# Performance work log

Hardware: AMD Instinct MI355X
Metric: run time of the kernel (lower is better)

Reference implementation:

```python
import jax, jax.numpy as jnp
import numpy as np

L, B, T, C, H, V = 4, 4, 1024, 1024, 16, 32000
DH = C // H
FF = 4 * C
IGNORE = 5
EPS = 1e-5


def setup_inputs() -> dict:
    key = jax.random.key(0)
    ks = jax.random.split(key, 12)
    s = 0.02
    return {
        "idx": jax.random.randint(ks[0], (B, T), 0, V),
        "targets": jax.random.randint(ks[1], (B, T), 0, V),
        "tok_emb": jax.random.normal(ks[2], (V, C), jnp.float32) * s,
        "pos_emb": jax.random.normal(ks[3], (T, C), jnp.float32) * s,
        "Wq": jax.random.normal(ks[4], (L, C, C), jnp.float32) * s,
        "Wk": jax.random.normal(ks[5], (L, C, C), jnp.float32) * s,
        "Wv": jax.random.normal(ks[6], (L, C, C), jnp.float32) * s,
        "Wo": jax.random.normal(ks[7], (L, C, C), jnp.float32) * s,
        "bo": jnp.zeros((L, C), jnp.float32),
        "ln1_g": jnp.ones((L, C), jnp.float32),
        "ln1_b": jnp.zeros((L, C), jnp.float32),
        "ln2_g": jnp.ones((L, C), jnp.float32),
        "ln2_b": jnp.zeros((L, C), jnp.float32),
        "W1": jax.random.normal(ks[8], (L, C, FF), jnp.float32) * s,
        "b1": jnp.zeros((L, FF), jnp.float32),
        "W2": jax.random.normal(ks[9], (L, FF, C), jnp.float32) * s,
        "b2": jnp.zeros((L, C), jnp.float32),
        "lnf_g": jnp.ones((C,), jnp.float32),
        "lnf_b": jnp.zeros((C,), jnp.float32),
        "Whead": jax.random.normal(ks[10], (C, V), jnp.float32) * s,
        "bhead": jnp.zeros((V,), jnp.float32),
    }


def _layernorm(x, g, b):
    mu = jnp.mean(x, axis=-1, keepdims=True)
    var = jnp.var(x, axis=-1, keepdims=True)
    return (x - mu) * jax.lax.rsqrt(var + EPS) * g + b


def _gpt_forward(idx, targets, tok_emb, pos_emb, Wq, Wk, Wv, Wo, bo,
                 ln1_g, ln1_b, ln2_g, ln2_b, W1, b1, W2, b2,
                 lnf_g, lnf_b, Whead, bhead):
    x = tok_emb[idx] + pos_emb[None, :, :]  # [B,T,C]
    causal = jnp.tril(jnp.ones((T, T), bool))
    for i in range(L):
        h = _layernorm(x, ln1_g[i], ln1_b[i])
        q = (h @ Wq[i]).reshape(B, T, H, DH)
        k = (h @ Wk[i]).reshape(B, T, H, DH)
        v = (h @ Wv[i]).reshape(B, T, H, DH)
        wei = jnp.einsum("bqhd,bkhd->bhqk", q, k) * (DH ** -0.5)
        wei = jnp.where(causal[None, None], wei, -jnp.inf)
        wei = jax.nn.softmax(wei, axis=-1)
        att = jnp.einsum("bhqk,bkhd->bqhd", wei, v).reshape(B, T, C)
        x = x + att @ Wo[i] + bo[i]
        h = _layernorm(x, ln2_g[i], ln2_b[i])
        x = x + jax.nn.gelu(h @ W1[i] + b1[i], approximate=False) @ W2[i] + b2[i]
    x = _layernorm(x, lnf_g, lnf_b)
    logits = x @ Whead + bhead  # [B,T,V]
    # cross-entropy with ignore_index=5
    lg = logits.reshape(B * T, V)
    tg = targets.reshape(B * T)
    logp = jax.nn.log_softmax(lg, axis=-1)
    nll = -jnp.take_along_axis(logp, tg[:, None], axis=-1)[:, 0]
    valid = (tg != IGNORE).astype(lg.dtype)
    loss = jnp.sum(nll * valid) / jnp.maximum(jnp.sum(valid), 1.0)
    return logits, loss


def reference(idx, targets, tok_emb, pos_emb, Wq, Wk, Wv, Wo, bo,
              ln1_g, ln1_b, ln2_g, ln2_b, W1, b1, W2, b2,
              lnf_g, lnf_b, Whead, bhead):
    return _gpt_forward(idx, targets, tok_emb, pos_emb, Wq, Wk, Wv, Wo, bo,
                        ln1_g, ln1_b, ln2_g, ln2_b, W1, b1, W2, b2,
                        lnf_g, lnf_b, Whead, bhead)
```

## Files before the change

### kernel.cpp

```cpp
#include <hip/hip_runtime.h>
#include <cstdint>
#include <cstddef>

#define Lx 4
#define Bx 4
#define Tx 1024
#define Cx 1024
#define Hx 16
#define DHx 64
#define FFx 4096
#define Vx 32000
#define BTx 4096

typedef __attribute__((ext_vector_type(8))) __bf16 bf16x8;
typedef __attribute__((ext_vector_type(4))) float f32x4;
typedef __attribute__((ext_vector_type(8))) short short8;

__device__ __forceinline__ float bflo(unsigned u){ return __builtin_bit_cast(float, u << 16); }
__device__ __forceinline__ float bfhi(unsigned u){ return __builtin_bit_cast(float, u & 0xffff0000u); }
__device__ __forceinline__ float bf2f(short s){ return bflo((unsigned)(unsigned short)s); }
__device__ __forceinline__ short f2bf(float f){
  unsigned u = __builtin_bit_cast(unsigned, f);
  u += 0x7fffu + ((u >> 16) & 1u);
  return (short)(u >> 16);
}

__device__ __forceinline__ void gload_lds16(const short* g, short* l){
  __builtin_amdgcn_global_load_lds(
      (const __attribute__((address_space(1))) unsigned int*)g,
      (__attribute__((address_space(3))) unsigned int*)l, 16, 0, 0);
}

__device__ __forceinline__ int xcd_swizzle(int orig, int nwg){
  const int q = nwg >> 3, r = nwg & 7;
  const int xcd = orig & 7, wg = orig >> 3;
  const int base = (xcd < r) ? xcd * (q + 1) : r * (q + 1) + (xcd - r) * q;
  return base + wg;
}

__global__ __launch_bounds__(256) void embed_kernel(
    const int* __restrict__ idx, const float* __restrict__ tok,
    const float* __restrict__ pos, float* __restrict__ x)
{
  const int bt = blockIdx.x;
  const int t  = bt & (Tx - 1);
  const int tid = threadIdx.x;
  const int tk = idx[bt];
  float4 a = *(const float4*)&tok[((size_t)tk << 10) + (tid << 2)];
  const float4 p = *(const float4*)&pos[((size_t)t << 10) + (tid << 2)];
  a.x += p.x; a.y += p.y; a.z += p.z; a.w += p.w;
  *(float4*)&x[((size_t)bt << 10) + (tid << 2)] = a;
}

__global__ __launch_bounds__(256) void ln_kernel(
    const float* __restrict__ x, const float* __restrict__ g,
    const float* __restrict__ b, short* __restrict__ out)
{
  const int row = blockIdx.x;
  const int tid = threadIdx.x;
  const float4 v = *(const float4*)&x[((size_t)row << 10) + (tid << 2)];
  float s  = v.x + v.y + v.z + v.w;
  float ss = v.x*v.x + v.y*v.y + v.z*v.z + v.w*v.w;
  #pragma unroll
  for (int off = 32; off >= 1; off >>= 1) {
    s  += __shfl_down(s, off);
    ss += __shfl_down(ss, off);
  }
  __shared__ float rs[4], rss[4];
  const int lane = tid & 63, w = tid >> 6;
  if (lane == 0) { rs[w] = s; rss[w] = ss; }
  __syncthreads();
  s  = rs[0] + rs[1] + rs[2] + rs[3];
  ss = rss[0] + rss[1] + rss[2] + rss[3];
  const float mu  = s * (1.0f / Cx);
  const float var = ss * (1.0f / Cx) - mu * mu;
  const float rstd = rsqrtf(var + 1e-5f);
  const float4 g4 = *(const float4*)&g[tid << 2];
  const float4 b4 = *(const float4*)&b[tid << 2];
  short4 o;
  o.x = f2bf((v.x - mu) * rstd * g4.x + b4.x);
  o.y = f2bf((v.y - mu) * rstd * g4.y + b4.y);
  o.z = f2bf((v.z - mu) * rstd * g4.z + b4.z);
  o.w = f2bf((v.w - mu) * rstd * g4.w + b4.w);
  *(short4*)&out[((size_t)row << 10) + (tid << 2)] = o;
}

__global__ __launch_bounds__(256) void wconv_kernel(
    const float* __restrict__ W, short* __restrict__ Wt, int K, int N)
{
  __shared__ float tile[32][33];
  const int n0 = blockIdx.x << 5, k0 = blockIdx.y << 5;
  const int tx = threadIdx.x & 31, ty = threadIdx.x >> 5;
  #pragma unroll
  for (int r = 0; r < 4; ++r)
    tile[ty + (r << 3)][tx] = __builtin_nontemporal_load(
        &W[(size_t)(k0 + ty + (r << 3)) * N + n0 + tx]);
  __syncthreads();
  #pragma unroll
  for (int r = 0; r < 4; ++r)
    Wt[(size_t)(n0 + ty + (r << 3)) * K + k0 + tx] = f2bf(tile[tx][ty + (r << 3)]);
}

template<int MODE>
__global__ __launch_bounds__(256) void gemm_kernel(
    const short* __restrict__ A, const short* __restrict__ Bt,
    const float* __restrict__ bias, const float* __restrict__ res,
    float* __restrict__ outF, short* __restrict__ outB, int N, int K)
{
  __shared__ __align__(16) short sA[128 * 32];
  __shared__ __align__(16) short sB[128 * 32];
  const int tid  = threadIdx.x;
  const int lane = tid & 63;
  const int wave = tid >> 6;
  const int bid  = xcd_swizzle((int)blockIdx.x, (int)gridDim.x);
  const int tm = (bid & 31) << 7;
  const int tn = (bid >> 5) << 7;
  const int wm = ((wave >> 1) & 1) << 6;
  const int wn = (wave & 1) << 6;

  f32x4 acc[4][4] = {};

  const int o1  = tid << 4;
  const int row = o1 >> 6;
  const int col = (o1 & 63) >> 1;
  const short* gA1 = A  + (size_t)(tm + row) * K + col;
  const short* gA2 = A  + (size_t)(tm + row + 64) * K + col;
  const short* gB1 = Bt + (size_t)(tn + row) * K + col;
  const short* gB2 = Bt + (size_t)(tn + row + 64) * K + col;
  short* lA1 = sA + (wave << 9);
  short* lA2 = sA + 2048 + (wave << 9);
  short* lB1 = sB + (wave << 9);
  short* lB2 = sB + 2048 + (wave << 9);

  for (int k0 = 0; k0 < K; k0 += 32) {
    gload_lds16(gA1 + k0, lA1);
    gload_lds16(gA2 + k0, lA2);
    gload_lds16(gB1 + k0, lB1);
    gload_lds16(gB2 + k0, lB2);
    __syncthreads();
    bf16x8 aF[4], bF[4];
    const int kb = (lane >> 4) << 3;
    const int rsel = lane & 15;
    #pragma unroll
    for (int m = 0; m < 4; ++m)
      aF[m] = *(const bf16x8*)&sA[(wm + m * 16 + rsel) * 32 + kb];
    #pragma unroll
    for (int n = 0; n < 4; ++n)
      bF[n] = *(const bf16x8*)&sB[(wn + n * 16 + rsel) * 32 + kb];
    #pragma unroll
    for (int m = 0; m < 4; ++m) {
      #pragma unroll
      for (int n = 0; n < 4; ++n)
        acc[m][n] = __builtin_amdgcn_mfma_f32_16x16x32_bf16(aF[m], bF[n], acc[m][n], 0, 0, 0);
    }
    __syncthreads();
  }

  const int r0 = (lane >> 4) << 2;
  const int c0 = lane & 15;
  #pragma unroll
  for (int m = 0; m < 4; ++m) {
    #pragma unroll
    for (int n = 0; n < 4; ++n) {
      #pragma unroll
      for (int r = 0; r < 4; ++r) {
        const int grow = tm + wm + m * 16 + r0 + r;
        const int gcol = tn + wn + n * 16 + c0;
        const float v = acc[m][n][r];
        const size_t o = (size_t)grow * N + gcol;
        outF[o] = res[o] + v + bias[gcol];
      }
    }
  }
}

#define GBAR() do { __builtin_amdgcn_sched_barrier(0); __builtin_amdgcn_s_barrier(); __builtin_amdgcn_sched_barrier(0); } while(0)
#define VM4 asm volatile("s_waitcnt vmcnt(4)" ::: "memory");
#define NOWAIT

#define PHASE(qq, dd, STAGES, ENDW) do { \
  aF[0][0] = RD_A(dd, qq, 0, 0); aF[0][1] = RD_A(dd, qq, 0, 1); \
  aF[1][0] = RD_A(dd, qq, 1, 0); aF[1][1] = RD_A(dd, qq, 1, 1); \
  STAGES \
  GBAR(); \
  asm volatile("s_waitcnt lgkmcnt(0)" ::: "memory"); \
  __builtin_amdgcn_sched_barrier(0); \
  __builtin_amdgcn_s_setprio(1); \
  _Pragma("unroll") \
  for (int ks = 0; ks < 2; ++ks) { \
    _Pragma("unroll") \
    for (int mf = 0; mf < 2; ++mf) { \
      _Pragma("unroll") \
      for (int nf = 0; nf < 4; ++nf) \
        acc[((qq) << 1) + mf][nf] = __builtin_amdgcn_mfma_f32_16x16x32_bf16( \
            aF[mf][ks], bF[nf][ks], acc[((qq) << 1) + mf][nf], 0, 0, 0); \
    } \
  } \
  __builtin_amdgcn_s_setprio(0); \
  ENDW \
  GBAR(); \
} while (0)

#define BLOAD(dd) do { \
  _Pragma("unroll") \
  for (int nf = 0; nf < 4; ++nf) { bF[nf][0] = RD_B(dd, nf, 0); bF[nf][1] = RD_B(dd, nf, 1); } \
} while (0)

template<int MODE>
__global__ __launch_bounds__(512, 2) void gemm256_kernel(
    const short* __restrict__ A, const short* __restrict__ Bt,
    const float* __restrict__ bias, float* __restrict__ outF,
    short* __restrict__ outB, int N, int K)
{
  __shared__ __align__(16) char lds[131072];
  const int tid  = threadIdx.x;
  const int lane = tid & 63;
  const int wid  = tid >> 6;
  const int wm   = wid >> 2;
  const int wn   = wid & 3;
  const int r15  = lane & 15;
  const int g4   = lane >> 4;
  const int bid  = xcd_swizzle((int)blockIdx.x, (int)gridDim.x);
  const int tm   = (bid & 15) << 8;
  const int tn   = (bid >> 4) << 8;
  const int NT   = K >> 6;
  const int NI   = NT >> 1;

  const int row0   = tid >> 3;
  const int innerE = ((tid & 7) ^ ((tid >> 3) & 7)) << 3;
  const int X0     = tid << 4;
  const short* srcA = A  + (size_t)(tm + row0) * K + innerE;
  const short* srcB = Bt + (size_t)(tn + row0) * K + innerE;
  const size_t h128K = (size_t)128 * K;
  const size_t r64K  = (size_t)64 * K;

  auto STAGE_A = [&](int t, int hh) {
    const short* s = srcA + (size_t)hh * h128K + (t << 6);
    char* d = lds + ((t & 1) << 15) + (hh << 14) + X0;
    gload_lds16(s, (short*)d);
    gload_lds16(s + r64K, (short*)(d + 8192));
  };
  auto STAGE_B = [&](int t, int hh) {
    const short* s = srcB + (size_t)hh * h128K + (t << 6);
    char* d = lds + 65536 + ((t & 1) << 15) + (hh << 14) + X0;
    gload_lds16(s, (short*)d);
    gload_lds16(s + r64K, (short*)(d + 8192));
  };

  const int arowb = (wm << 7) + r15;
  const int bcolb = (wn << 6) + r15;
  const int kchnk = g4 << 4;
  auto RD_A = [&](int d, int q, int mf, int ks) -> bf16x8 {
    const int row = arowb + (q << 5) + (mf << 4);
    return *(const bf16x8*)(lds + (d << 15) + (row << 7) +
                            ((((ks) << 6) + kchnk) ^ ((row & 7) << 4)));
  };
  auto RD_B = [&](int d, int nf, int ks) -> bf16x8 {
    const int colc = bcolb + (nf << 4);
    return *(const bf16x8*)(lds + 65536 + (d << 15) + (colc << 7) +
                            ((((ks) << 6) + kchnk) ^ ((colc & 7) << 4)));
  };

  f32x4 acc[8][4] = {};

  STAGE_A(0, 0); STAGE_A(0, 1); STAGE_B(0, 0); STAGE_B(0, 1);
  STAGE_B(1, 0); STAGE_B(1, 1);
  VM4
  GBAR();

  for (int i = 0; i < NI; ++i) {
    const int t1 = 2 * i + 1;
    const int ta = (2 * i + 2 < NT) ? 2 * i + 2 : NT - 2;
    const int tb = (2 * i + 3 < NT) ? 2 * i + 3 : NT - 1;
    bf16x8 aF[2][2], bF[4][2];
    BLOAD(0);
    PHASE(0, 0, { STAGE_A(t1, 0); },                  NOWAIT);
    PHASE(1, 0, { STAGE_A(t1, 1); STAGE_B(ta, 0); },  NOWAIT);
    PHASE(2, 0, { STAGE_B(ta, 1); },                  NOWAIT);
    PHASE(3, 0, { },                                  VM4);
    BLOAD(1);
    PHASE(0, 1, { STAGE_A(ta, 0); },                  NOWAIT);
    PHASE(1, 1, { STAGE_A(ta, 1); STAGE_B(tb, 0); },  NOWAIT);
    PHASE(2, 1, { STAGE_B(tb, 1); },                  NOWAIT);
    PHASE(3, 1, { },                                  VM4);
  }

  #pragma unroll
  for (int m8 = 0; m8 < 8; ++m8) {
    #pragma unroll
    for (int nf = 0; nf < 4; ++nf) {
      #pragma unroll
      for (int r = 0; r < 4; ++r) {
        const int grow = tm + (wm << 7) + (m8 << 4) + (g4 << 2) + r;
        const int gcol = tn + (wn << 6) + (nf << 4) + r15;
        const float v = acc[m8][nf][r];
        if constexpr (MODE == 0) {
          const int which = gcol >> 10;
          const int cc = gcol & 1023;
          const int b = grow >> 10, t = grow & 1023;
          const int hh = cc >> 6, d = cc & 63;
          outB[(size_t)which * (BTx * Cx) +
               ((size_t)((((b << 4) + hh) << 10) + t) << 6) + d] = f2bf(v);
        } else if constexpr (MODE == 2) {
          const float t2 = v + bias[gcol];
          const float gl = 0.5f * t2 * (1.0f + erff(t2 * 0.7071067811865475f));
          outB[(size_t)grow * N + gcol] = f2bf(gl);
        } else {
          outF[(size_t)grow * N + gcol] = v + bias[gcol];
        }
      }
    }
  }
}

__global__ __launch_bounds__(256) void fattn_kernel(
    const short* __restrict__ q, const short* __restrict__ k,
    const short* __restrict__ v, short* __restrict__ att)
{
  __shared__ __align__(16) short sQ[4096];
  __shared__ __align__(16) short sK[4096];
  __shared__ __align__(16) short sVT[4096];
  __shared__ __align__(16) short sP[4][1024];

  const int tid  = threadIdx.x;
  const int lane = tid & 63;
  const int w    = tid >> 6;
  const int r15  = lane & 15;
  const int g4   = lane >> 4;
  const int bid  = xcd_swizzle((int)blockIdx.x, (int)gridDim.x);
  const int qt   = bid & 15;
  const int bh   = bid >> 4;

  const char* Qb = (const char*)(q + ((size_t)bh << 16)) + ((size_t)qt << 13);
  const char* Kb = (const char*)(k + ((size_t)bh << 16));
  const char* Vb = (const char*)(v + ((size_t)bh << 16));

  const int X0  = tid << 4;
  const int X1  = X0 + 4096;
  const int sw0 = X0 ^ (((X0 >> 7) & 7) << 4);
  const int sw1 = X1 ^ (((X1 >> 7) & 7) << 4);
  const int ldsOff0 = (w << 10);
  const int ldsOff1 = (w << 10) + 4096;

  gload_lds16((const short*)(Qb + sw0), (short*)((char*)sQ + ldsOff0));
  gload_lds16((const short*)(Qb + sw1), (short*)((char*)sQ + ldsOff1));
  __syncthreads();
  bf16x8 aQ[2];
  {
    const int qrow = (w << 4) + r15;
    const int base = qrow * 128 + (g4 << 4);
    const int sz = (qrow & 7) << 4;
    aQ[0] = *(const bf16x8*)((char*)sQ + ((base     ) ^ sz));
    aQ[1] = *(const bf16x8*)((char*)sQ + ((base + 64) ^ sz));
  }

  const int vdh  = (lane & 31) << 1;
  const int vkv0 = (((w << 1) + (lane >> 5)) << 3);
  const int vb0  = (vdh * 128 + vkv0 * 2)       ^ ((vdh & 7) << 4);
  const int vb1  = ((vdh + 1) * 128 + vkv0 * 2) ^ (((vdh + 1) & 7) << 4);

  float m[4] = {-3e38f, -3e38f, -3e38f, -3e38f};
  float l[4] = {0.f, 0.f, 0.f, 0.f};
  f32x4 acc_o[4] = {};
  const int qrow_g0 = (qt << 6) + (w << 4) + (g4 << 2);

  for (int kt = 0; kt <= qt; ++kt) {
    __syncthreads();
    const char* Kt = Kb + ((size_t)kt << 13);
    gload_lds16((const short*)(Kt + sw0), (short*)((char*)sK + ldsOff0));
    gload_lds16((const short*)(Kt + sw1), (short*)((char*)sK + ldsOff1));
    {
      const char* Vt = Vb + ((size_t)kt << 13);
      unsigned uv[8];
      #pragma unroll
      for (int j = 0; j < 8; ++j)
        uv[j] = *(const unsigned*)(Vt + ((vkv0 + j) << 7) + (vdh << 1));
      short8 plo, phi;
      #pragma unroll
      for (int j = 0; j < 8; ++j) {
        plo[j] = (short)(uv[j] & 0xffffu);
        phi[j] = (short)(uv[j] >> 16);
      }
      *(short8*)((char*)sVT + vb0) = plo;
      *(short8*)((char*)sVT + vb1) = phi;
    }
    __syncthreads();

    f32x4 s[4] = {};
    #pragma unroll
    for (int f = 0; f < 4; ++f) {
      const int kv = (f << 4) + r15;
      const int kb = kv * 128 + (g4 << 4);
      const int sz = (kv & 7) << 4;
      const bf16x8 b0 = *(const bf16x8*)((char*)sK + ((kb     ) ^ sz));
      const bf16x8 b1 = *(const bf16x8*)((char*)sK + ((kb + 64) ^ sz));
      s[f] = __builtin_amdgcn_mfma_f32_16x16x32_bf16(aQ[0], b0, s[f], 0, 0, 0);
      s[f] = __builtin_amdgcn_mfma_f32_16x16x32_bf16(aQ[1], b1, s[f], 0, 0, 0);
    }
    #pragma unroll
    for (int f = 0; f < 4; ++f) {
      #pragma unroll
      for (int r = 0; r < 4; ++r) {
        float sv = s[f][r] * 0.125f;
        if ((kt << 6) + (f << 4) + r15 > qrow_g0 + r) sv = -3e38f;
        s[f][r] = sv;
      }
    }
    #pragma unroll
    for (int r = 0; r < 4; ++r) {
      float mx = fmaxf(fmaxf(s[0][r], s[1][r]), fmaxf(s[2][r], s[3][r]));
      mx = fmaxf(mx, __shfl_xor(mx, 1));
      mx = fmaxf(mx, __shfl_xor(mx, 2));
      mx = fmaxf(mx, __shfl_xor(mx, 4));
      mx = fmaxf(mx, __shfl_xor(mx, 8));
      const float mn = fmaxf(m[r], mx);
      const float e  = __expf(m[r] - mn);
      float sum = 0.f;
      #pragma unroll
      for (int f = 0; f < 4; ++f) {
        const float p = __expf(s[f][r] - mn);
        s[f][r] = p; sum += p;
      }
      sum += __shfl_xor(sum, 1);
      sum += __shfl_xor(sum, 2);
      sum += __shfl_xor(sum, 4);
      sum += __shfl_xor(sum, 8);
      l[r] = l[r] * e + sum;
      m[r] = mn;
      acc_o[0][r] *= e; acc_o[1][r] *= e; acc_o[2][r] *= e; acc_o[3][r] *= e;
    }
    short* Pw = sP[w];
    #pragma unroll
    for (int f = 0; f < 4; ++f) {
      #pragma unroll
      for (int r = 0; r < 4; ++r) {
        const int prow = (g4 << 2) + r;
        const int byte = prow * 128 + (((f << 4) + r15) << 1);
        *(short*)((char*)Pw + (byte ^ ((prow & 7) << 4))) = f2bf(s[f][r]);
      }
    }
    #pragma unroll
    for (int ks = 0; ks < 2; ++ks) {
      const int ab = r15 * 128 + (ks << 6) + (g4 << 4);
      const bf16x8 aP = *(const bf16x8*)((char*)Pw + (ab ^ ((r15 & 7) << 4)));
      #pragma unroll
      for (int f = 0; f < 4; ++f) {
        const int dh = (f << 4) + r15;
        const int bb = dh * 128 + (ks << 6) + (g4 << 4);
        const bf16x8 bV = *(const bf16x8*)((char*)sVT + (bb ^ ((dh & 7) << 4)));
        acc_o[f] = __builtin_amdgcn_mfma_f32_16x16x32_bf16(aP, bV, acc_o[f], 0, 0, 0);
      }
    }
  }

  const int b = bh >> 4, hh = bh & 15;
  #pragma unroll
  for (int f = 0; f < 4; ++f) {
    #pragma unroll
    for (int r = 0; r < 4; ++r) {
      const int qg = qrow_g0 + r;
      const int dh = (f << 4) + r15;
      att[((size_t)((b << 10) + qg) << 10) + (hh << 6) + dh] = f2bf(acc_o[f][r] / l[r]);
    }
  }
}

__global__ void ce_zero_kernel(float* accum){ accum[0] = 0.0f; accum[1] = 0.0f; }

__global__ __launch_bounds__(256) void ce_row_kernel(
    const float* __restrict__ logits, const int* __restrict__ tgt, float* __restrict__ accum)
{
  const int row = blockIdx.x;
  const float* lg = logits + (size_t)row * Vx;
  const int tid = threadIdx.x;
  float m = -1e30f, ssum = 0.0f;
  for (int i = tid; i < Vx; i += 256) {
    const float v2 = __builtin_nontemporal_load(&lg[i]);
    const float nm = fmaxf(m, v2);
    ssum = ssum * __expf(m - nm) + __expf(v2 - nm);
    m = nm;
  }
  #pragma unroll
  for (int off = 32; off >= 1; off >>= 1) {
    const float om = __shfl_down(m, off), os = __shfl_down(ssum, off);
    const float nm = fmaxf(m, om);
    ssum = ssum * __expf(m - nm) + os * __expf(om - nm);
    m = nm;
  }
  __shared__ float ms[4], sss[4];
  if ((tid & 63) == 0) { ms[tid >> 6] = m; sss[tid >> 6] = ssum; }
  __syncthreads();
  if (tid == 0) {
    float M = ms[0], S = sss[0];
    #pragma unroll
    for (int i = 1; i < 4; ++i) {
      const float nm = fmaxf(M, ms[i]);
      S = S * __expf(M - nm) + sss[i] * __expf(ms[i] - nm);
      M = nm;
    }
    const int tg = tgt[row];
    if (tg != 5) {
      const float lt = lg[tg];
      const float nll = -(lt - M - logf(S));
      atomicAdd(&accum[0], nll);
      atomicAdd(&accum[1], 1.0f);
    }
  }
}

__global__ void ce_final_kernel(const float* __restrict__ accum, float* __restrict__ out)
{
  out[131072000ull] = accum[0] / fmaxf(accum[1], 1.0f);
}

extern "C" void kernel_launch(void* const* d_in, const int* in_sizes, int n_in,
                              void* d_out, int out_size, void* d_ws, size_t ws_size,
                              hipStream_t stream)
{
  const int*   idx     = (const int*)d_in[0];
  const int*   targets = (const int*)d_in[1];
  const float* tok_emb = (const float*)d_in[2];
  const float* pos_emb = (const float*)d_in[3];
  const float* Wq      = (const float*)d_in[4];
  const float* Wk      = (const float*)d_in[5];
  const float* Wv      = (const float*)d_in[6];
  const float* Wo      = (const float*)d_in[7];
  const float* bo      = (const float*)d_in[8];
  const float* ln1_g   = (const float*)d_in[9];
  const float* ln1_b   = (const float*)d_in[10];
  const float* ln2_g   = (const float*)d_in[11];
  const float* ln2_b   = (const float*)d_in[12];
  const float* W1      = (const float*)d_in[13];
  const float* b1      = (const float*)d_in[14];
  const float* W2      = (const float*)d_in[15];
  const float* b2      = (const float*)d_in[16];
  const float* lnf_g   = (const float*)d_in[17];
  const float* lnf_b   = (const float*)d_in[18];
  const float* Whead   = (const float*)d_in[19];
  const float* bhead   = (const float*)d_in[20];
  float* out = (float*)d_out;

  char* ws = (char*)d_ws;
  size_t off = 0;
  auto alloc = [&](size_t bytes) -> char* {
    char* p = ws + off;
    off += (bytes + 255) & ~(size_t)255;
    return p;
  };
  float* x    = (float*)alloc((size_t)BTx * Cx * 4);
  short* h    = (short*)alloc((size_t)BTx * Cx * 2);
  char*  blk  = ws + off;
  short* qb   = (short*)alloc((size_t)BTx * Cx * 2);
  short* kb   = (short*)alloc((size_t)BTx * Cx * 2);
  short* vb   = (short*)alloc((size_t)BTx * Cx * 2);
  short* attb = (short*)alloc((size_t)BTx * Cx * 2);
  short* ffb  = (short*)alloc((size_t)BTx * FFx * 2);
  short* wheadT = (short*)blk;
  short* wqkvT = (short*)alloc((size_t)3 * Cx * Cx * 2);
  short* woT  = (short*)alloc((size_t)Cx * Cx * 2);
  short* w1T  = (short*)alloc((size_t)Cx * FFx * 2);
  short* w2T  = (short*)alloc((size_t)FFx * Cx * 2);
  float* accum = (float*)alloc(256);
  if (ws_size < off) return;
  short* wqT = wqkvT;
  short* wkT = wqkvT + (size_t)Cx * Cx;
  short* wvT = wqkvT + (size_t)2 * Cx * Cx;

  embed_kernel<<<BTx, 256, 0, stream>>>(idx, tok_emb, pos_emb, x);
  ce_zero_kernel<<<1, 1, 0, stream>>>(accum);

  for (int i = 0; i < Lx; ++i) {
    const size_t wo_off = (size_t)i * Cx * Cx;
    const size_t w1_off = (size_t)i * Cx * FFx;
    wconv_kernel<<<dim3(Cx / 32, Cx / 32), 256, 0, stream>>>(Wq + wo_off, wqT, Cx, Cx);
    wconv_kernel<<<dim3(Cx / 32, Cx / 32), 256, 0, stream>>>(Wk + wo_off, wkT, Cx, Cx);
    wconv_kernel<<<dim3(Cx / 32, Cx / 32), 256, 0, stream>>>(Wv + wo_off, wvT, Cx, Cx);
    wconv_kernel<<<dim3(Cx / 32, Cx / 32), 256, 0, stream>>>(Wo + wo_off, woT, Cx, Cx);
    wconv_kernel<<<dim3(FFx / 32, Cx / 32), 256, 0, stream>>>(W1 + w1_off, w1T, Cx, FFx);
    wconv_kernel<<<dim3(Cx / 32, FFx / 32), 256, 0, stream>>>(W2 + w1_off, w2T, FFx, Cx);

    ln_kernel<<<BTx, 256, 0, stream>>>(x, ln1_g + i * Cx, ln1_b + i * Cx, h);
    gemm256_kernel<0><<<16 * 12, 512, 0, stream>>>(h, wqkvT, nullptr, nullptr, qb, 3 * Cx, Cx);
    fattn_kernel<<<Bx * Hx * (Tx / 64), 256, 0, stream>>>(qb, kb, vb, attb);
    gemm_kernel<1><<<(BTx / 128) * (Cx / 128), 256, 0, stream>>>(attb, woT, bo + i * Cx, x, x, nullptr, Cx, Cx);

    ln_kernel<<<BTx, 256, 0, stream>>>(x, ln2_g + i * Cx, ln2_b + i * Cx, h);
    gemm256_kernel<2><<<16 * 16, 512, 0, stream>>>(h, w1T, b1 + i * FFx, nullptr, ffb, FFx, Cx);
    gemm_kernel<1><<<(BTx / 128) * (Cx / 128), 256, 0, stream>>>(ffb, w2T, b2 + i * Cx, x, x, nullptr, Cx, FFx);
  }

  ln_kernel<<<BTx, 256, 0, stream>>>(x, lnf_g, lnf_b, h);
  wconv_kernel<<<dim3(Vx / 32, Cx / 32), 256, 0, stream>>>(Whead, wheadT, Cx, Vx);
  gemm256_kernel<3><<<16 * 125, 512, 0, stream>>>(h, wheadT, bhead, out, nullptr, Vx, Cx);

  ce_row_kernel<<<BTx, 256, 0, stream>>>(out, targets, accum);
  ce_final_kernel<<<1, 1, 0, stream>>>(accum, out);
}
```

Baseline: 1.750 ms.

## Fuse cross-entropy partial log-sum-exp into LM-head GEMM epilogue

The LM-head GEMM epilogue now computes a per-row max and sum-of-exp for each 256-column tile and writes them to a small partials buffer. A light kernel merges the 125 partials per row and computes the NLL, and a single-block kernel reduces the loss deterministically without atomics. The logits are staged through LDS and written with vectorized nontemporal stores instead of scalar stores. This removes the second full pass over the 4096x32000 float logits in the old cross-entropy kernel, at the cost of extra epilogue work, more barriers, and reusing weight buffers as scratch space.

```diff
diff --git a/kernel.cpp b/kernel.cpp
--- a/kernel.cpp
+++ b/kernel.cpp
@@ -210,7 +210,7 @@
 __global__ __launch_bounds__(512, 2) void gemm256_kernel(
     const short* __restrict__ A, const short* __restrict__ Bt,
     const float* __restrict__ bias, float* __restrict__ outF,
-    short* __restrict__ outB, int N, int K)
+    short* __restrict__ outB, float2* __restrict__ cep, int N, int K)
 {
   __shared__ __align__(16) char lds[131072];
   const int tid  = threadIdx.x;
@@ -285,28 +285,98 @@
     PHASE(3, 1, { },                                  VM4);
   }
 
-  #pragma unroll
-  for (int m8 = 0; m8 < 8; ++m8) {
-    #pragma unroll
-    for (int nf = 0; nf < 4; ++nf) {
+  if constexpr (MODE == 3) {
+    const int nb = tn >> 8;
+    float bb4[4];
+    #pragma unroll
+    for (int nf = 0; nf < 4; ++nf) bb4[nf] = bias[tn + (wn << 6) + (nf << 4) + r15];
+    #pragma unroll
+    for (int m8 = 0; m8 < 8; ++m8)
+      #pragma unroll
+      for (int nf = 0; nf < 4; ++nf)
+        #pragma unroll
+        for (int r = 0; r < 4; ++r) acc[m8][nf][r] += bb4[nf];
+
+    float2* cepart = (float2*)lds;
+    #pragma unroll
+    for (int m8 = 0; m8 < 8; ++m8) {
       #pragma unroll
       for (int r = 0; r < 4; ++r) {
-        const int grow = tm + (wm << 7) + (m8 << 4) + (g4 << 2) + r;
-        const int gcol = tn + (wn << 6) + (nf << 4) + r15;
-        const float v = acc[m8][nf][r];
-        if constexpr (MODE == 0) {
-          const int which = gcol >> 10;
-          const int cc = gcol & 1023;
-          const int b = grow >> 10, t = grow & 1023;
-          const int hh = cc >> 6, d = cc & 63;
-          outB[(size_t)which * (BTx * Cx) +
-               ((size_t)((((b << 4) + hh) << 10) + t) << 6) + d] = f2bf(v);
-        } else if constexpr (MODE == 2) {
-          const float t2 = v + bias[gcol];
-          const float gl = 0.5f * t2 * (1.0f + erff(t2 * 0.7071067811865475f));
-          outB[(size_t)grow * N + gcol] = f2bf(gl);
-        } else {
-          outF[(size_t)grow * N + gcol] = v + bias[gcol];
+        float mx = fmaxf(fmaxf(acc[m8][0][r], acc[m8][1][r]),
+                         fmaxf(acc[m8][2][r], acc[m8][3][r]));
+        mx = fmaxf(mx, __shfl_xor(mx, 1));
+        mx = fmaxf(mx, __shfl_xor(mx, 2));
+        mx = fmaxf(mx, __shfl_xor(mx, 4));
+        mx = fmaxf(mx, __shfl_xor(mx, 8));
+        float sm = __expf(acc[m8][0][r] - mx) + __expf(acc[m8][1][r] - mx)
+                 + __expf(acc[m8][2][r] - mx) + __expf(acc[m8][3][r] - mx);
+        sm += __shfl_xor(sm, 1);
+        sm += __shfl_xor(sm, 2);
+        sm += __shfl_xor(sm, 4);
+        sm += __shfl_xor(sm, 8);
+        if (r15 == 0) {
+          float2 v2; v2.x = mx; v2.y = sm;
+          cepart[(wn << 8) + (wm << 7) + (m8 << 4) + (g4 << 2) + r] = v2;
+        }
+      }
+    }
+    __syncthreads();
+    if (tid < 256) {
+      float M = -3e38f, S = 0.f;
+      #pragma unroll
+      for (int w2 = 0; w2 < 4; ++w2) {
+        const float2 ms = cepart[(w2 << 8) + tid];
+        const float nm = fmaxf(M, ms.x);
+        S = S * __expf(M - nm) + ms.y * __expf(ms.x - nm);
+        M = nm;
+      }
+      float2 o2; o2.x = M; o2.y = S;
+      cep[(size_t)(tm + tid) * 125 + nb] = o2;
+    }
+
+    float* tbuf = (float*)(lds + 32768);
+    const int rrow = lane >> 4;
+    const int c4   = (lane & 15) << 2;
+    #pragma unroll
+    for (int m8 = 0; m8 < 8; ++m8) {
+      __syncthreads();
+      #pragma unroll
+      for (int nf = 0; nf < 4; ++nf)
+        #pragma unroll
+        for (int r = 0; r < 4; ++r)
+          tbuf[(wid << 10) + (((g4 << 2) + r) << 6) + (nf << 4) + r15] = acc[m8][nf][r];
+      __syncthreads();
+      #pragma unroll
+      for (int p = 0; p < 4; ++p) {
+        const int rw = (p << 2) + rrow;
+        const f32x4 vv = *(const f32x4*)&tbuf[(wid << 10) + (rw << 6) + c4];
+        const int grow2 = tm + (wm << 7) + (m8 << 4) + rw;
+        const int gcol2 = tn + (wn << 6) + c4;
+        __builtin_nontemporal_store(vv, (f32x4*)&outF[(size_t)grow2 * N + gcol2]);
+      }
+    }
+  } else {
+    #pragma unroll
+    for (int m8 = 0; m8 < 8; ++m8) {
+      #pragma unroll
+      for (int nf = 0; nf < 4; ++nf) {
+        #pragma unroll
+        for (int r = 0; r < 4; ++r) {
+          const int grow = tm + (wm << 7) + (m8 << 4) + (g4 << 2) + r;
+          const int gcol = tn + (wn << 6) + (nf << 4) + r15;
+          const float v = acc[m8][nf][r];
+          if constexpr (MODE == 0) {
+            const int which = gcol >> 10;
+            const int cc = gcol & 1023;
+            const int b = grow >> 10, t = grow & 1023;
+            const int hh = cc >> 6, d = cc & 63;
+            outB[(size_t)which * (BTx * Cx) +
+                 ((size_t)((((b << 4) + hh) << 10) + t) << 6) + d] = f2bf(v);
+          } else {
+            const float t2 = v + bias[gcol];
+            const float gl = 0.5f * t2 * (1.0f + erff(t2 * 0.7071067811865475f));
+            outB[(size_t)grow * N + gcol] = f2bf(gl);
+          }
         }
       }
     }
@@ -465,52 +535,61 @@
   }
 }
 
-__global__ void ce_zero_kernel(float* accum){ accum[0] = 0.0f; accum[1] = 0.0f; }
-
-__global__ __launch_bounds__(256) void ce_row_kernel(
-    const float* __restrict__ logits, const int* __restrict__ tgt, float* __restrict__ accum)
-{
-  const int row = blockIdx.x;
-  const float* lg = logits + (size_t)row * Vx;
+__global__ __launch_bounds__(256) void ce_lse_kernel(
+    const float2* __restrict__ part, const float* __restrict__ logits,
+    const int* __restrict__ tgt, float2* __restrict__ nll)
+{
+  const int row  = blockIdx.x * 4 + (threadIdx.x >> 6);
+  const int lane = threadIdx.x & 63;
+  float M = -3e38f, S = 0.f;
+  #pragma unroll
+  for (int p = 0; p < 2; ++p) {
+    const int i = lane + (p << 6);
+    if (i < 125) {
+      const float2 ms = part[(size_t)row * 125 + i];
+      const float nm = fmaxf(M, ms.x);
+      S = S * __expf(M - nm) + ms.y * __expf(ms.x - nm);
+      M = nm;
+    }
+  }
+  #pragma unroll
+  for (int off = 32; off >= 1; off >>= 1) {
+    const float oM = __shfl_xor(M, off), oS = __shfl_xor(S, off);
+    const float nm = fmaxf(M, oM);
+    S = S * __expf(M - nm) + oS * __expf(oM - nm);
+    M = nm;
+  }
+  if (lane == 0) {
+    const int tg = tgt[row];
+    float v = 0.f, cnt = 0.f;
+    if (tg != 5) {
+      const float lt = logits[(size_t)row * Vx + tg];
+      v = -(lt - M - logf(S));
+      cnt = 1.f;
+    }
+    float2 o2; o2.x = v; o2.y = cnt;
+    nll[row] = o2;
+  }
+}
+
+__global__ __launch_bounds__(256) void ce_sum_kernel(
+    const float2* __restrict__ nll, float* __restrict__ out)
+{
   const int tid = threadIdx.x;
-  float m = -1e30f, ssum = 0.0f;
-  for (int i = tid; i < Vx; i += 256) {
-    const float v2 = __builtin_nontemporal_load(&lg[i]);
-    const float nm = fmaxf(m, v2);
-    ssum = ssum * __expf(m - nm) + __expf(v2 - nm);
-    m = nm;
-  }
-  #pragma unroll
-  for (int off = 32; off >= 1; off >>= 1) {
-    const float om = __shfl_down(m, off), os = __shfl_down(ssum, off);
-    const float nm = fmaxf(m, om);
-    ssum = ssum * __expf(m - nm) + os * __expf(om - nm);
-    m = nm;
-  }
-  __shared__ float ms[4], sss[4];
-  if ((tid & 63) == 0) { ms[tid >> 6] = m; sss[tid >> 6] = ssum; }
+  float s = 0.f, c = 0.f;
+  #pragma unroll
+  for (int i = 0; i < 16; ++i) {
+    const float2 v = nll[tid * 16 + i];
+    s += v.x; c += v.y;
+  }
+  __shared__ float ls[256], lc[256];
+  ls[tid] = s; lc[tid] = c;
   __syncthreads();
-  if (tid == 0) {
-    float M = ms[0], S = sss[0];
-    #pragma unroll
-    for (int i = 1; i < 4; ++i) {
-      const float nm = fmaxf(M, ms[i]);
-      S = S * __expf(M - nm) + sss[i] * __expf(ms[i] - nm);
-      M = nm;
-    }
-    const int tg = tgt[row];
-    if (tg != 5) {
-      const float lt = lg[tg];
-      const float nll = -(lt - M - logf(S));
-      atomicAdd(&accum[0], nll);
-      atomicAdd(&accum[1], 1.0f);
-    }
-  }
-}
-
-__global__ void ce_final_kernel(const float* __restrict__ accum, float* __restrict__ out)
-{
-  out[131072000ull] = accum[0] / fmaxf(accum[1], 1.0f);
+  for (int off = 128; off >= 1; off >>= 1) {
+    if (tid < off) { ls[tid] += ls[tid + off]; lc[tid] += lc[tid + off]; }
+    __syncthreads();
+  }
+  if (tid == 0) out[131072000ull] = ls[0] / fmaxf(lc[0], 1.0f);
 }
 
 extern "C" void kernel_launch(void* const* d_in, const int* in_sizes, int n_in,
@@ -560,14 +639,14 @@
   short* woT  = (short*)alloc((size_t)Cx * Cx * 2);
   short* w1T  = (short*)alloc((size_t)Cx * FFx * 2);
   short* w2T  = (short*)alloc((size_t)FFx * Cx * 2);
-  float* accum = (float*)alloc(256);
   if (ws_size < off) return;
   short* wqT = wqkvT;
   short* wkT = wqkvT + (size_t)Cx * Cx;
   short* wvT = wqkvT + (size_t)2 * Cx * Cx;
+  float2* part = (float2*)wqkvT;
+  float2* nllb = (float2*)woT;
 
   embed_kernel<<<BTx, 256, 0, stream>>>(idx, tok_emb, pos_emb, x);
-  ce_zero_kernel<<<1, 1, 0, stream>>>(accum);
 
   for (int i = 0; i < Lx; ++i) {
     const size_t wo_off = (size_t)i * Cx * Cx;
@@ -580,19 +659,19 @@
     wconv_kernel<<<dim3(Cx / 32, FFx / 32), 256, 0, stream>>>(W2 + w1_off, w2T, FFx, Cx);
 
     ln_kernel<<<BTx, 256, 0, stream>>>(x, ln1_g + i * Cx, ln1_b + i * Cx, h);
-    gemm256_kernel<0><<<16 * 12, 512, 0, stream>>>(h, wqkvT, nullptr, nullptr, qb, 3 * Cx, Cx);
+    gemm256_kernel<0><<<16 * 12, 512, 0, stream>>>(h, wqkvT, nullptr, nullptr, qb, nullptr, 3 * Cx, Cx);
     fattn_kernel<<<Bx * Hx * (Tx / 64), 256, 0, stream>>>(qb, kb, vb, attb);
     gemm_kernel<1><<<(BTx / 128) * (Cx / 128), 256, 0, stream>>>(attb, woT, bo + i * Cx, x, x, nullptr, Cx, Cx);
 
     ln_kernel<<<BTx, 256, 0, stream>>>(x, ln2_g + i * Cx, ln2_b + i * Cx, h);
-    gemm256_kernel<2><<<16 * 16, 512, 0, stream>>>(h, w1T, b1 + i * FFx, nullptr, ffb, FFx, Cx);
+    gemm256_kernel<2><<<16 * 16, 512, 0, stream>>>(h, w1T, b1 + i * FFx, nullptr, ffb, nullptr, FFx, Cx);
     gemm_kernel<1><<<(BTx / 128) * (Cx / 128), 256, 0, stream>>>(ffb, w2T, b2 + i * Cx, x, x, nullptr, Cx, FFx);
   }
 
   ln_kernel<<<BTx, 256, 0, stream>>>(x, lnf_g, lnf_b, h);
   wconv_kernel<<<dim3(Vx / 32, Cx / 32), 256, 0, stream>>>(Whead, wheadT, Cx, Vx);
-  gemm256_kernel<3><<<16 * 125, 512, 0, stream>>>(h, wheadT, bhead, out, nullptr, Vx, Cx);
-
-  ce_row_kernel<<<BTx, 256, 0, stream>>>(out, targets, accum);
-  ce_final_kernel<<<1, 1, 0, stream>>>(accum, out);
-}
+  gemm256_kernel<3><<<16 * 125, 512, 0, stream>>>(h, wheadT, bhead, out, nullptr, part, Vx, Cx);
+
+  ce_lse_kernel<<<BTx / 4, 256, 0, stream>>>(part, out, targets, nllb);
+  ce_sum_kernel<<<1, 256, 0, stream>>>(nllb, out);
+}
```

After: 1.594 ms. -8.9%, faster.
